# Optimization experiments

Measured on AMD Instinct MI355X. Metric: run time of the kernel, lower is better.

Reference implementation:

```python
import jax, jax.numpy as jnp
import numpy as np

B, C, CI, H, W = 8, 256, 128, 64, 64
EPS = 1e-5

def conv1x1(x, w, b):
    # x: [B,C,H,W], w: [O,C], b: [O]
    return jnp.einsum('bchw,oc->bohw', x, w) + b[None, :, None, None]

def avgpool2(x):
    b, c, h, w = x.shape
    return x.reshape(b, c, h // 2, 2, w // 2, 2).mean(axis=(3, 5))

def setup_inputs() -> dict:
    key = jax.random.key(0)
    ks = jax.random.split(key, 16)
    s = lambda fan: 1.0 / np.sqrt(fan)
    inp = {
        'q': jax.random.normal(ks[0], (B, C, H, W), jnp.float32),
        'k': jax.random.normal(ks[1], (B, C, H, W), jnp.float32),
        'v': jax.random.normal(ks[2], (B, C, H, W), jnp.float32),
        'Wg':  jax.random.normal(ks[3], (CI, C), jnp.float32) * s(C),
        'bg':  jax.random.normal(ks[4], (CI,), jnp.float32) * s(C),
        'Wth': jax.random.normal(ks[5], (CI, C), jnp.float32) * s(C),
        'bth': jax.random.normal(ks[6], (CI,), jnp.float32) * s(C),
        'Wph': jax.random.normal(ks[7], (CI, C), jnp.float32) * s(C),
        'bph': jax.random.normal(ks[8], (CI,), jnp.float32) * s(C),
        'Ww':  jax.random.normal(ks[9], (C, CI), jnp.float32) * s(CI),
        'bw':  jax.random.normal(ks[10], (C,), jnp.float32) * s(CI),
        'gamma': jax.random.normal(ks[11], (C,), jnp.float32) * 0.1 + 1.0,
        'beta':  jax.random.normal(ks[12], (C,), jnp.float32) * 0.1,
        'mean':  jax.random.normal(ks[13], (C,), jnp.float32) * 0.1,
        'var':   jax.random.uniform(ks[14], (C,), jnp.float32, 0.5, 1.5),
    }
    return inp

def reference(q, k, v, Wg, bg, Wth, bth, Wph, bph, Ww, bw, gamma, beta, mean, var):
    b = q.shape[0]
    # g branch on v, phi branch on q: 1x1 conv then 2x2 avg-pool (sub_sample)
    g_x = avgpool2(conv1x1(v, Wg, bg)).reshape(b, CI, -1)            # [B,CI,M]
    g_x = g_x.transpose(0, 2, 1)                                      # [B,M,CI]
    theta_x = conv1x1(k, Wth, bth).reshape(b, CI, -1).transpose(0, 2, 1)  # [B,N,CI]
    phi_x = avgpool2(conv1x1(q, Wph, bph)).reshape(b, CI, -1)        # [B,CI,M]
    f = jnp.einsum('bnc,bcm->bnm', theta_x, phi_x)                   # [B,N,M]
    f_div_C = jax.nn.softmax(f, axis=-1)
    y = jnp.einsum('bnm,bmc->bnc', f_div_C, g_x)                     # [B,N,CI]
    y = y.transpose(0, 2, 1).reshape(b, CI, H, W)
    W_y = conv1x1(y, Ww, bw)
    # BatchNorm2d (inference form)
    W_y = (W_y - mean[None, :, None, None]) * (gamma[None, :, None, None]
            * jax.lax.rsqrt(var + EPS)[None, :, None, None]) + beta[None, :, None, None]
    return W_y + v
```

## Files before the change

kernel.cpp:

```cpp
#include <hip/hip_runtime.h>
#include <cstddef>

typedef unsigned short u16;
typedef unsigned int u32;
typedef __attribute__((ext_vector_type(8))) __bf16 bf16x8;
typedef __attribute__((ext_vector_type(4))) float f32x4;

constexpr int kB = 8, kC = 256, kCI = 128, kN = 4096, kM = 1024;
constexpr float kEPS = 1e-5f;
constexpr float kLOG2E = 1.44269504088896f;

__device__ __forceinline__ u16 f2bf(float f) {
    u32 u = __float_as_uint(f);
    u32 r = (u + 0x7fffu + ((u >> 16) & 1u)) >> 16;
    return (u16)r;
}

__global__ __launch_bounds__(256) void prep_kernel(const float* __restrict__ Wth,
                                                   const float* __restrict__ bth,
                                                   const float* __restrict__ Wph,
                                                   const float* __restrict__ Wg,
                                                   const float* __restrict__ Ww,
                                                   const float* __restrict__ bw,
                                                   const float* __restrict__ gamma,
                                                   const float* __restrict__ beta,
                                                   const float* __restrict__ mean,
                                                   const float* __restrict__ var,
                                                   u16* __restrict__ Wthb,
                                                   u16* __restrict__ Wphb,
                                                   u16* __restrict__ Wgb,
                                                   u16* __restrict__ Wwsb,
                                                   float* __restrict__ bb,
                                                   float* __restrict__ bthl) {
    int idx = blockIdx.x * 256 + threadIdx.x;
    if (idx < 32768) {
        Wthb[idx] = f2bf(Wth[idx] * kLOG2E);
        if (idx < kCI) bthl[idx] = bth[idx] * kLOG2E;
    } else if (idx < 65536) {
        int j = idx - 32768; Wphb[j] = f2bf(Wph[j]);
    } else if (idx < 98304) {
        int j = idx - 65536; Wgb[j] = f2bf(Wg[j]);
    } else {
        int j = idx - 98304;
        int co = j >> 7;
        float sc = gamma[co] * rsqrtf(var[co] + kEPS);
        Wwsb[j] = f2bf(Ww[j] * sc);
        if ((j & 127) == 0) bb[co] = (bw[co] - mean[co]) * sc + beta[co];
    }
}

template <int POOL>
__device__ __forceinline__ void conv_body(const float* __restrict__ x,
                                          const u16* __restrict__ Wb,
                                          const float* __restrict__ bias,
                                          u16* __restrict__ out, int Mn,
                                          int cmajor, int b, int n0,
                                          u16* x_lds) {
    int t = threadIdx.x;
    int w = t >> 6, lane = t & 63, l15 = lane & 15, quad = lane >> 4;
    int px = t & 63, cb8 = t >> 6;

    for (int cc8 = 0; cc8 < 8; cc8++) {
        int cb = cb8 * 8 + cc8;
        int c0 = cb * 8;
        float f[8];
        if (POOL) {
            int p = n0 + px, ph_ = p >> 5, pw_ = p & 31;
#pragma unroll
            for (int j = 0; j < 8; j++) {
                const float* src = x + ((size_t)(b * kC + c0 + j) * 64
                                        + 2 * ph_) * 64 + 2 * pw_;
                float2 a = *(const float2*)src;
                float2 b2 = *(const float2*)(src + 64);
                f[j] = 0.25f * (a.x + a.y + b2.x + b2.y);
            }
        } else {
#pragma unroll
            for (int j = 0; j < 8; j++)
                f[j] = x[(size_t)(b * kC + c0 + j) * Mn + n0 + px];
        }
        uint4 pk;
        pk.x = (u32)f2bf(f[0]) | ((u32)f2bf(f[1]) << 16);
        pk.y = (u32)f2bf(f[2]) | ((u32)f2bf(f[3]) << 16);
        pk.z = (u32)f2bf(f[4]) | ((u32)f2bf(f[5]) << 16);
        pk.w = (u32)f2bf(f[6]) | ((u32)f2bf(f[7]) << 16);
        *(uint4*)&x_lds[px * 256 + ((cb ^ (px & 7)) * 8)] = pk;
    }
    __syncthreads();

    f32x4 acc[8];
#pragma unroll
    for (int i = 0; i < 8; i++) acc[i] = (f32x4){0.f, 0.f, 0.f, 0.f};

    int rpx = w * 16 + l15;
#pragma unroll
    for (int ks = 0; ks < 8; ks++) {
        bf16x8 xf = *(const bf16x8*)&x_lds[rpx * 256 +
                                           (((ks * 4 + quad) ^ (rpx & 7)) * 8)];
#pragma unroll
        for (int ct = 0; ct < 8; ct++) {
            bf16x8 wf = *(const bf16x8*)&Wb[(ct * 16 + l15) * kC + ks * 32 + quad * 8];
            if (cmajor)
                acc[ct] = __builtin_amdgcn_mfma_f32_16x16x32_bf16(xf, wf, acc[ct], 0, 0, 0);
            else
                acc[ct] = __builtin_amdgcn_mfma_f32_16x16x32_bf16(wf, xf, acc[ct], 0, 0, 0);
        }
    }

    if (cmajor == 0) {
        int opx = n0 + w * 16 + l15;
#pragma unroll
        for (int ct = 0; ct < 8; ct++) {
            int ci0 = ct * 16 + quad * 4;
            uint2 pk;
            pk.x = (u32)f2bf(acc[ct][0] + bias[ci0 + 0]) |
                   ((u32)f2bf(acc[ct][1] + bias[ci0 + 1]) << 16);
            pk.y = (u32)f2bf(acc[ct][2] + bias[ci0 + 2]) |
                   ((u32)f2bf(acc[ct][3] + bias[ci0 + 3]) << 16);
            *(uint2*)&out[(size_t)(b * Mn + opx) * kCI + ci0] = pk;
        }
    } else {
        int opx = n0 + w * 16 + quad * 4;
#pragma unroll
        for (int ct = 0; ct < 8; ct++) {
            int ci = ct * 16 + l15;
            float bs = bias[ci];
            uint2 pk;
            pk.x = (u32)f2bf(acc[ct][0] + bs) | ((u32)f2bf(acc[ct][1] + bs) << 16);
            pk.y = (u32)f2bf(acc[ct][2] + bs) | ((u32)f2bf(acc[ct][3] + bs) << 16);
            *(uint2*)&out[(size_t)(b * kCI + ci) * Mn + opx] = pk;
        }
    }
}

__global__ __launch_bounds__(256, 4) void convs_kernel(const float* __restrict__ q,
                                                       const float* __restrict__ k,
                                                       const float* __restrict__ v,
                                                       const u16* __restrict__ Wthb,
                                                       const u16* __restrict__ Wphb,
                                                       const u16* __restrict__ Wgb,
                                                       const float* __restrict__ bthl,
                                                       const float* __restrict__ bph,
                                                       const float* __restrict__ bg,
                                                       u16* __restrict__ theta,
                                                       u16* __restrict__ phi,
                                                       u16* __restrict__ g) {
    __shared__ __align__(16) u16 x_lds[64 * 256];
    int bx = blockIdx.x, b = blockIdx.y;
    if (bx < 64) {
        conv_body<0>(k, Wthb, bthl, theta, kN, 0, b, bx * 64, x_lds);
    } else {
        int z = (bx >= 80);
        int n0 = (z ? (bx - 80) : (bx - 64)) * 64;
        conv_body<1>(z ? v : q, z ? Wgb : Wphb, z ? bg : bph, z ? g : phi,
                     kM, z, b, n0, x_lds);
    }
}

__global__ __launch_bounds__(256) void attn_kernel(const u16* __restrict__ theta,
                                                   const u16* __restrict__ phi,
                                                   const u16* __restrict__ g,
                                                   u16* __restrict__ y) {
    __shared__ __align__(16) u16 ph_lds[8192];
    __shared__ __align__(16) u16 g_lds[8192];
    __shared__ __align__(16) u16 p_lds[4096];

    int t = threadIdx.x, b = blockIdx.y, n0 = blockIdx.x * 64;
    int w = t >> 6, lane = t & 63, l15 = lane & 15, quad = lane >> 4;
    int sw = (l15 >> 1) & 3;

    bf16x8 thf[4];
    const u16* thB = theta + ((size_t)(b * kN) + n0 + w * 16 + l15) * kCI;
#pragma unroll
    for (int ks = 0; ks < 4; ks++)
        thf[ks] = *(const bf16x8*)&thB[ks * 32 + quad * 8];

    f32x4 oacc[8];
#pragma unroll
    for (int ct = 0; ct < 8; ct++) oacc[ct] = (f32x4){0.f, 0.f, 0.f, 0.f};
    float m_ = -1e30f, l_ = 0.f;

    const u16* phB = phi + (size_t)b * kM * kCI;
    const u16* gB  = g   + (size_t)b * kCI * kM;
    u16* pw = p_lds + w * 1024;

    for (int c0 = 0; c0 < kM; c0 += 64) {
        __syncthreads();
#pragma unroll
        for (int it = 0; it < 4; it++) {
            int u = t + 256 * it;
            int row = u >> 4, cb = u & 15;
            *(uint4*)&ph_lds[(cb >> 2) * 2048 + row * 32 + (((cb & 3) ^ ((row >> 1) & 3)) * 8)] =
                *(const uint4*)&phB[(size_t)(c0 + row) * kCI + cb * 8];
        }
#pragma unroll
        for (int it = 0; it < 4; it++) {
            int u = t + 256 * it;
            int ci = u >> 3, mb = u & 7;
            *(uint4*)&g_lds[(mb >> 2) * 4096 + ci * 32 + (((mb & 3) ^ ((ci >> 1) & 3)) * 8)] =
                *(const uint4*)&gB[(size_t)ci * kM + c0 + mb * 8];
        }
        __syncthreads();

        f32x4 sacc[4];
#pragma unroll
        for (int mt = 0; mt < 4; mt++) sacc[mt] = (f32x4){0.f, 0.f, 0.f, 0.f};
#pragma unroll
        for (int ks = 0; ks < 4; ks++)
#pragma unroll
            for (int mt = 0; mt < 4; mt++) {
                bf16x8 a = *(const bf16x8*)&ph_lds[ks * 2048 + (mt * 16 + l15) * 32 +
                                                   ((quad ^ sw) * 8)];
                sacc[mt] = __builtin_amdgcn_mfma_f32_16x16x32_bf16(a, thf[ks], sacc[mt], 0, 0, 0);
            }

        float mc = -1e30f;
#pragma unroll
        for (int mt = 0; mt < 4; mt++)
#pragma unroll
            for (int r = 0; r < 4; r++) mc = fmaxf(mc, sacc[mt][r]);
        mc = fmaxf(mc, __shfl_xor(mc, 16, 64));
        mc = fmaxf(mc, __shfl_xor(mc, 32, 64));
        if (__any(mc > m_ + 8.0f)) {
            float mn = fmaxf(m_, mc);
            float al = exp2f(m_ - mn);
            m_ = mn;
            l_ *= al;
#pragma unroll
            for (int ct = 0; ct < 8; ct++)
#pragma unroll
                for (int r = 0; r < 4; r++) oacc[ct][r] *= al;
        }
        float rs = 0.f;
#pragma unroll
        for (int mt = 0; mt < 4; mt++)
#pragma unroll
            for (int r = 0; r < 4; r++) {
                float p = exp2f(sacc[mt][r] - m_);
                sacc[mt][r] = p;
                rs += p;
            }
        l_ += rs;

#pragma unroll
        for (int mt = 0; mt < 4; mt++)
#pragma unroll
            for (int h = 0; h < 2; h++) {
                u32 d = (u32)f2bf(sacc[mt][2 * h]) | ((u32)f2bf(sacc[mt][2 * h + 1]) << 16);
                int m = mt * 16 + quad * 4 + 2 * h;
                int frag = m >> 5;
                int kblk = ((m >> 3) & 3);
                int j = (quad & 1) * 4 + 2 * h;
                *(u32*)&pw[frag * 512 + l15 * 32 + ((kblk ^ sw) * 8) + j] = d;
            }

#pragma unroll
        for (int ks2 = 0; ks2 < 2; ks2++) {
            bf16x8 bfrag = *(const bf16x8*)&pw[ks2 * 512 + l15 * 32 + ((quad ^ sw) * 8)];
#pragma unroll
            for (int ct = 0; ct < 8; ct++) {
                bf16x8 a = *(const bf16x8*)&g_lds[ks2 * 4096 + (ct * 16 + l15) * 32 +
                                                  ((quad ^ sw) * 8)];
                oacc[ct] = __builtin_amdgcn_mfma_f32_16x16x32_bf16(a, bfrag, oacc[ct], 0, 0, 0);
            }
        }
    }

    l_ += __shfl_xor(l_, 16, 64);
    l_ += __shfl_xor(l_, 32, 64);
    float inv = 1.0f / l_;
    int n = n0 + w * 16 + l15;
    u16* yr = y + ((size_t)(b * kN) + n) * kCI + quad * 4;
#pragma unroll
    for (int ct = 0; ct < 8; ct++) {
        uint2 pk;
        pk.x = (u32)f2bf(oacc[ct][0] * inv) | ((u32)f2bf(oacc[ct][1] * inv) << 16);
        pk.y = (u32)f2bf(oacc[ct][2] * inv) | ((u32)f2bf(oacc[ct][3] * inv) << 16);
        *(uint2*)&yr[ct * 16] = pk;
    }
}

__global__ __launch_bounds__(256) void final_kernel(const u16* __restrict__ y,
                                                    const u16* __restrict__ Wws,
                                                    const float* __restrict__ bb,
                                                    const float* __restrict__ v,
                                                    float* __restrict__ out) {
    __shared__ __align__(16) u16 y_lds[64 * 136];
    int t = threadIdx.x, b = blockIdx.y, n0 = blockIdx.x * 64;
    int z = blockIdx.z;
    int w = t >> 6, lane = t & 63, l15 = lane & 15, quad = lane >> 4;

#pragma unroll
    for (int i = 0; i < 4; i++) {
        int u = t + 256 * i;
        int row = u >> 4, blk = u & 15;
        *(uint4*)&y_lds[row * 136 + blk * 8] =
            *(const uint4*)&y[(size_t)(b * kN + n0 + row) * kCI + blk * 8];
    }
    __syncthreads();

    bf16x8 af[4];
#pragma unroll
    for (int ks = 0; ks < 4; ks++)
        af[ks] = *(const bf16x8*)&y_lds[(w * 16 + l15) * 136 + ks * 32 + quad * 8];

#pragma unroll
    for (int ct = 0; ct < 8; ct++) {
        int co = z * 128 + ct * 16 + l15;
        f32x4 a = (f32x4){0.f, 0.f, 0.f, 0.f};
#pragma unroll
        for (int ks = 0; ks < 4; ks++) {
            bf16x8 bf = *(const bf16x8*)&Wws[(size_t)co * kCI + ks * 32 + quad * 8];
            a = __builtin_amdgcn_mfma_f32_16x16x32_bf16(af[ks], bf, a, 0, 0, 0);
        }
        float bbv = bb[co];
        size_t base = (size_t)(b * kC + co) * kN + n0 + w * 16 + quad * 4;
        float4 vv = *(const float4*)&v[base];
        float4 ov;
        ov.x = a[0] + bbv + vv.x;
        ov.y = a[1] + bbv + vv.y;
        ov.z = a[2] + bbv + vv.z;
        ov.w = a[3] + bbv + vv.w;
        *(float4*)&out[base] = ov;
    }
}

extern "C" void kernel_launch(void* const* d_in, const int* in_sizes, int n_in,
                              void* d_out, int out_size, void* d_ws, size_t ws_size,
                              hipStream_t stream) {
    (void)in_sizes; (void)n_in; (void)out_size; (void)ws_size;
    const float* q     = (const float*)d_in[0];
    const float* k     = (const float*)d_in[1];
    const float* v     = (const float*)d_in[2];
    const float* Wg    = (const float*)d_in[3];
    const float* bg    = (const float*)d_in[4];
    const float* Wth   = (const float*)d_in[5];
    const float* bth   = (const float*)d_in[6];
    const float* Wph   = (const float*)d_in[7];
    const float* bph   = (const float*)d_in[8];
    const float* Ww    = (const float*)d_in[9];
    const float* bw    = (const float*)d_in[10];
    const float* gamma = (const float*)d_in[11];
    const float* beta  = (const float*)d_in[12];
    const float* mean  = (const float*)d_in[13];
    const float* var   = (const float*)d_in[14];
    float* out = (float*)d_out;

    u16* wsu = (u16*)d_ws;
    u16*   theta = wsu;
    u16*   phi   = theta + 4194304;
    u16*   gbuf  = phi + 1048576;
    u16*   ybuf  = gbuf + 1048576;
    u16*   Wthb  = ybuf + 4194304;
    u16*   Wphb  = Wthb + 32768;
    u16*   Wgb   = Wphb + 32768;
    u16*   Wwsb  = Wgb + 32768;
    float* bbuf  = (float*)(Wwsb + 32768);
    float* bthl  = bbuf + 256;

    prep_kernel<<<dim3(512), 256, 0, stream>>>(Wth, bth, Wph, Wg, Ww, bw, gamma, beta,
                                               mean, var, Wthb, Wphb, Wgb, Wwsb,
                                               bbuf, bthl);
    convs_kernel<<<dim3(96, 8), 256, 0, stream>>>(q, k, v, Wthb, Wphb, Wgb,
                                                  bthl, bph, bg, theta, phi, gbuf);
    attn_kernel<<<dim3(64, 8), 256, 0, stream>>>(theta, phi, gbuf, ybuf);
    final_kernel<<<dim3(64, 8, 2), 256, 0, stream>>>(ybuf, Wwsb, bbuf, v, out);
}
```

Before: 254.9 us.

## Double-buffer attention loads via direct global-to-LDS and fuse output conv epilogue

The attention kernel now stages phi and g chunks into double-buffered LDS using global_load_lds, so the load for the next chunk overlaps compute on the current one. It also fuses the final 1x1 conv, BN bias and residual add into the attention epilogue, which removes the y round-trip through global memory and one kernel launch. In exchange, LDS use doubles, and the fused epilogue runs all 256 output channels per block on only 512 blocks, where the separate final kernel used 1024 blocks, so there is less parallelism in that phase.

```diff
diff --git a/kernel.cpp b/kernel.cpp
--- a/kernel.cpp
+++ b/kernel.cpp
@@ -7,6 +7,7 @@
 typedef __attribute__((ext_vector_type(4))) float f32x4;
 
 constexpr int kB = 8, kC = 256, kCI = 128, kN = 4096, kM = 1024;
+constexpr int kCH = 64, kNCH = kM / kCH;
 constexpr float kEPS = 1e-5f;
 constexpr float kLOG2E = 1.44269504088896f;
 
@@ -14,6 +15,12 @@
     u32 u = __float_as_uint(f);
     u32 r = (u + 0x7fffu + ((u >> 16) & 1u)) >> 16;
     return (u16)r;
+}
+
+__device__ __forceinline__ void gload_lds16(const u16* g, u16* l) {
+    __builtin_amdgcn_global_load_lds(
+        (const __attribute__((address_space(1))) void*)g,
+        (__attribute__((address_space(3))) void*)l, 16, 0, 0);
 }
 
 __global__ __launch_bounds__(256) void prep_kernel(const float* __restrict__ Wth,
@@ -160,9 +167,12 @@
 __global__ __launch_bounds__(256) void attn_kernel(const u16* __restrict__ theta,
                                                    const u16* __restrict__ phi,
                                                    const u16* __restrict__ g,
-                                                   u16* __restrict__ y) {
-    __shared__ __align__(16) u16 ph_lds[8192];
-    __shared__ __align__(16) u16 g_lds[8192];
+                                                   const u16* __restrict__ Wws,
+                                                   const float* __restrict__ bb,
+                                                   const float* __restrict__ v,
+                                                   float* __restrict__ out) {
+    __shared__ __align__(16) u16 ph_lds[2][8192];
+    __shared__ __align__(16) u16 g_lds[2][8192];
     __shared__ __align__(16) u16 p_lds[4096];
 
     int t = threadIdx.x, b = blockIdx.y, n0 = blockIdx.x * 64;
@@ -184,23 +194,34 @@
     const u16* gB  = g   + (size_t)b * kCI * kM;
     u16* pw = p_lds + w * 1024;
 
-    for (int c0 = 0; c0 < kM; c0 += 64) {
+    auto STAGE = [&](int buf, int ch) {
+        int c0 = ch * kCH;
+#pragma unroll
+        for (int i = 0; i < 4; i++) {
+            int W = t + 256 * i;
+            int ks = W >> 8, m = (W >> 2) & 63, sl = W & 3;
+            int cb = (ks << 2) | (sl ^ ((m >> 1) & 3));
+            gload_lds16(phB + (size_t)(c0 + m) * kCI + cb * 8,
+                        &ph_lds[buf][(w * 64 + i * 256) * 8]);
+        }
+#pragma unroll
+        for (int i = 0; i < 4; i++) {
+            int W = t + 256 * i;
+            int ks2 = W >> 9, ci = (W >> 2) & 127, sl = W & 3;
+            int mb = (ks2 << 2) | (sl ^ ((ci >> 1) & 3));
+            gload_lds16(gB + (size_t)ci * kM + c0 + mb * 8,
+                        &g_lds[buf][(w * 64 + i * 256) * 8]);
+        }
+    };
+
+    STAGE(0, 0);
+
+    for (int ch = 0; ch < kNCH; ++ch) {
+        asm volatile("s_waitcnt vmcnt(0)" ::: "memory");
         __syncthreads();
-#pragma unroll
-        for (int it = 0; it < 4; it++) {
-            int u = t + 256 * it;
-            int row = u >> 4, cb = u & 15;
-            *(uint4*)&ph_lds[(cb >> 2) * 2048 + row * 32 + (((cb & 3) ^ ((row >> 1) & 3)) * 8)] =
-                *(const uint4*)&phB[(size_t)(c0 + row) * kCI + cb * 8];
-        }
-#pragma unroll
-        for (int it = 0; it < 4; it++) {
-            int u = t + 256 * it;
-            int ci = u >> 3, mb = u & 7;
-            *(uint4*)&g_lds[(mb >> 2) * 4096 + ci * 32 + (((mb & 3) ^ ((ci >> 1) & 3)) * 8)] =
-                *(const uint4*)&gB[(size_t)ci * kM + c0 + mb * 8];
-        }
-        __syncthreads();
+        if (ch + 1 < kNCH) STAGE((ch + 1) & 1, ch + 1);
+        const u16* phb = ph_lds[ch & 1];
+        const u16* glb = g_lds[ch & 1];
 
         f32x4 sacc[4];
 #pragma unroll
@@ -209,8 +230,8 @@
         for (int ks = 0; ks < 4; ks++)
 #pragma unroll
             for (int mt = 0; mt < 4; mt++) {
-                bf16x8 a = *(const bf16x8*)&ph_lds[ks * 2048 + (mt * 16 + l15) * 32 +
-                                                   ((quad ^ sw) * 8)];
+                bf16x8 a = *(const bf16x8*)&phb[ks * 2048 + (mt * 16 + l15) * 32 +
+                                                ((quad ^ sw) * 8)];
                 sacc[mt] = __builtin_amdgcn_mfma_f32_16x16x32_bf16(a, thf[ks], sacc[mt], 0, 0, 0);
             }
 
@@ -259,8 +280,8 @@
             bf16x8 bfrag = *(const bf16x8*)&pw[ks2 * 512 + l15 * 32 + ((quad ^ sw) * 8)];
 #pragma unroll
             for (int ct = 0; ct < 8; ct++) {
-                bf16x8 a = *(const bf16x8*)&g_lds[ks2 * 4096 + (ct * 16 + l15) * 32 +
-                                                  ((quad ^ sw) * 8)];
+                bf16x8 a = *(const bf16x8*)&glb[ks2 * 4096 + (ct * 16 + l15) * 32 +
+                                                ((quad ^ sw) * 8)];
                 oacc[ct] = __builtin_amdgcn_mfma_f32_16x16x32_bf16(a, bfrag, oacc[ct], 0, 0, 0);
             }
         }
@@ -269,44 +290,27 @@
     l_ += __shfl_xor(l_, 16, 64);
     l_ += __shfl_xor(l_, 32, 64);
     float inv = 1.0f / l_;
-    int n = n0 + w * 16 + l15;
-    u16* yr = y + ((size_t)(b * kN) + n) * kCI + quad * 4;
+
+    __syncthreads();
+    u16* y_lds = &ph_lds[0][0];
+    int nrow = w * 16 + l15;
 #pragma unroll
     for (int ct = 0; ct < 8; ct++) {
         uint2 pk;
         pk.x = (u32)f2bf(oacc[ct][0] * inv) | ((u32)f2bf(oacc[ct][1] * inv) << 16);
         pk.y = (u32)f2bf(oacc[ct][2] * inv) | ((u32)f2bf(oacc[ct][3] * inv) << 16);
-        *(uint2*)&yr[ct * 16] = pk;
-    }
-}
-
-__global__ __launch_bounds__(256) void final_kernel(const u16* __restrict__ y,
-                                                    const u16* __restrict__ Wws,
-                                                    const float* __restrict__ bb,
-                                                    const float* __restrict__ v,
-                                                    float* __restrict__ out) {
-    __shared__ __align__(16) u16 y_lds[64 * 136];
-    int t = threadIdx.x, b = blockIdx.y, n0 = blockIdx.x * 64;
-    int z = blockIdx.z;
-    int w = t >> 6, lane = t & 63, l15 = lane & 15, quad = lane >> 4;
-
-#pragma unroll
-    for (int i = 0; i < 4; i++) {
-        int u = t + 256 * i;
-        int row = u >> 4, blk = u & 15;
-        *(uint4*)&y_lds[row * 136 + blk * 8] =
-            *(const uint4*)&y[(size_t)(b * kN + n0 + row) * kCI + blk * 8];
+        *(uint2*)&y_lds[nrow * 136 + ct * 16 + quad * 4] = pk;
     }
     __syncthreads();
 
     bf16x8 af[4];
 #pragma unroll
     for (int ks = 0; ks < 4; ks++)
-        af[ks] = *(const bf16x8*)&y_lds[(w * 16 + l15) * 136 + ks * 32 + quad * 8];
-
-#pragma unroll
-    for (int ct = 0; ct < 8; ct++) {
-        int co = z * 128 + ct * 16 + l15;
+        af[ks] = *(const bf16x8*)&y_lds[nrow * 136 + ks * 32 + quad * 8];
+
+#pragma unroll
+    for (int ct = 0; ct < 16; ct++) {
+        int co = ct * 16 + l15;
         f32x4 a = (f32x4){0.f, 0.f, 0.f, 0.f};
 #pragma unroll
         for (int ks = 0; ks < 4; ks++) {
@@ -350,8 +354,7 @@
     u16*   theta = wsu;
     u16*   phi   = theta + 4194304;
     u16*   gbuf  = phi + 1048576;
-    u16*   ybuf  = gbuf + 1048576;
-    u16*   Wthb  = ybuf + 4194304;
+    u16*   Wthb  = gbuf + 1048576;
     u16*   Wphb  = Wthb + 32768;
     u16*   Wgb   = Wphb + 32768;
     u16*   Wwsb  = Wgb + 32768;
@@ -363,6 +366,5 @@
                                                bbuf, bthl);
     convs_kernel<<<dim3(96, 8), 256, 0, stream>>>(q, k, v, Wthb, Wphb, Wgb,
                                                   bthl, bph, bg, theta, phi, gbuf);
-    attn_kernel<<<dim3(64, 8), 256, 0, stream>>>(theta, phi, gbuf, ybuf);
-    final_kernel<<<dim3(64, 8, 2), 256, 0, stream>>>(ybuf, Wwsb, bbuf, v, out);
-}
+    attn_kernel<<<dim3(64, 8), 256, 0, stream>>>(theta, phi, gbuf, Wwsb, bbuf, v, out);
+}
```

New measurement: 225.2 us. 1.13x faster.
